# Optimization experiments

Hardware: AMD Instinct MI355X
Metric: run time of the kernel (lower is better)

Reference implementation:

```python
import jax, jax.numpy as jnp
import numpy as np

B, S, D, H = 16, 1024, 768, 12
HD = D // H  # head_dim = 64

def setup_inputs() -> dict:
    key = jax.random.key(0)
    ks = jax.random.split(key, 6)
    s = 1.0 / np.sqrt(D)
    return {
        "z": jax.random.normal(ks[0], (B, S, D), dtype=jnp.float32),
        "W_q": jax.random.normal(ks[1], (D, D), dtype=jnp.float32) * s,
        "W_k": jax.random.normal(ks[2], (D, D), dtype=jnp.float32) * s,
        "W_v": jax.random.normal(ks[3], (D, D), dtype=jnp.float32) * s,
        "W_o": jax.random.normal(ks[4], (D, D), dtype=jnp.float32) * s,
        "b_o": jax.random.normal(ks[5], (D,), dtype=jnp.float32) * s,
    }

def reference(z, W_q, W_k, W_v, W_o, b_o):
    batch, seq, _ = z.shape
    # torch Linear: y = x @ W.T
    q = (z @ W_q.T).reshape(batch, seq, H, HD).transpose(0, 2, 1, 3)  # [B,H,S,hd]
    k = (z @ W_k.T).reshape(batch, seq, H, HD).transpose(0, 2, 1, 3)
    v = (z @ W_v.T).reshape(batch, seq, H, HD).transpose(0, 2, 1, 3)
    scores = jnp.einsum("bhqd,bhkd->bhqk", q, k) / np.sqrt(HD)
    attn = jax.nn.softmax(scores, axis=-1)
    ctx = jnp.einsum("bhqk,bhkd->bhqd", attn, v)  # [B,H,S,hd]
    ctx = ctx.transpose(0, 2, 1, 3).reshape(batch, seq, D)
    return ctx @ W_o.T + b_o
```

## Files before the change

### kernel.cpp

```cpp
#include <hip/hip_runtime.h>
#include <hip/hip_bf16.h>


typedef __attribute__((ext_vector_type(4))) float f32x4;
typedef __attribute__((ext_vector_type(16))) float f32x16;
typedef __attribute__((ext_vector_type(8))) __bf16 bf16x8;
typedef __attribute__((ext_vector_type(4))) unsigned int u32x4;

#if __has_builtin(__builtin_amdgcn_exp2f)
#define EXP2F __builtin_amdgcn_exp2f
#else
#define EXP2F exp2f
#endif

__device__ __forceinline__ unsigned short f2bf(float f) {
  union { float f; unsigned u; } v; v.f = f;
  unsigned r = v.u + 0x7FFFu + ((v.u >> 16) & 1u);
  return (unsigned short)(r >> 16);
}

__device__ __forceinline__ unsigned cvtpk(float a, float b) {
  unsigned r;
  asm("v_cvt_pk_bf16_f32 %0, %1, %2" : "=v"(r) : "v"(a), "v"(b));
  return r;
}

__device__ __forceinline__ void gl_lds16(const void* g, void* l) {
  __builtin_amdgcn_global_load_lds(
      (const __attribute__((address_space(1))) void*)g,
      (__attribute__((address_space(3))) void*)l, 16, 0, 0);
}

__global__ void cvt_f32_bf16(const float* __restrict__ in,
                             unsigned short* __restrict__ out, int n4) {
  int i = blockIdx.x * blockDim.x + threadIdx.x;
  int stride = gridDim.x * blockDim.x;
  for (; i < n4; i += stride) {
    float4 v = ((const float4*)in)[i];
    ushort4 o;
    o.x = f2bf(v.x); o.y = f2bf(v.y); o.z = f2bf(v.z); o.w = f2bf(v.w);
    ((ushort4*)out)[i] = o;
  }
}

__global__ void cvt4_f32_bf16(const float* __restrict__ i0, const float* __restrict__ i1,
                              const float* __restrict__ i2, const float* __restrict__ i3,
                              unsigned short* __restrict__ o0, unsigned short* __restrict__ o1,
                              unsigned short* __restrict__ o2, unsigned short* __restrict__ o3,
                              int n4) {
  const float* in = (blockIdx.y == 0) ? i0 : (blockIdx.y == 1) ? i1 : (blockIdx.y == 2) ? i2 : i3;
  unsigned short* out = (blockIdx.y == 0) ? o0 : (blockIdx.y == 1) ? o1 : (blockIdx.y == 2) ? o2 : o3;
  int i = blockIdx.x * blockDim.x + threadIdx.x;
  int stride = gridDim.x * blockDim.x;
  for (; i < n4; i += stride) {
    float4 v = ((const float4*)in)[i];
    ushort4 o;
    o.x = f2bf(v.x); o.y = f2bf(v.y); o.z = f2bf(v.z); o.w = f2bf(v.w);
    ((ushort4*)out)[i] = o;
  }
}

__global__ __launch_bounds__(256) void qkv_gemm(
    const unsigned short* __restrict__ A,
    const unsigned short* __restrict__ Wq,
    const unsigned short* __restrict__ Wk,
    const unsigned short* __restrict__ Wv,
    unsigned short* __restrict__ Qo,
    unsigned short* __restrict__ Ko,
    unsigned short* __restrict__ Vt) {
  __shared__ unsigned short As[2][128 * 64];
  __shared__ unsigned short Bs[2][128 * 64];
  const int bid = blockIdx.x;
  const int xcd = bid & 7, slot = bid >> 3;
  const int mt = xcd * 16 + slot / 18;
  const int rem = slot % 18;
  const int which = rem / 6;
  const int nt = rem % 6;
  const unsigned short* __restrict__ W =
      (which == 0) ? Wq : (which == 1) ? Wk : Wv;
  const int m0 = mt * 128;
  const int n0 = nt * 128;
  const int tid = threadIdx.x;
  const int lane = tid & 63;
  const int l15 = lane & 15, lg = lane >> 4;
  const int w = tid >> 6;
  const int wm = (w >> 1) * 64, wn = (w & 1) * 64;

  const int srow = tid >> 3;
  const int scg8 = (((tid & 7) ^ (srow & 7)) << 3);

#define QSTAGE(bi, kt)                                                         \
  do {                                                                         \
    _Pragma("unroll") for (int it = 0; it < 4; ++it) {                         \
      int row = srow + it * 32;                                                \
      int dst = (row * 8 + (tid & 7)) * 8;                                     \
      gl_lds16(A + (size_t)(m0 + row) * 768 + (kt) + scg8, &As[bi][dst]);      \
      gl_lds16(W + (size_t)(n0 + row) * 768 + (kt) + scg8, &Bs[bi][dst]);      \
    }                                                                          \
  } while (0)

  f32x4 acc[4][4] = {};
  const int rxf = l15 & 7;

  QSTAGE(0, 0);
  for (int kt = 0; kt < 768; kt += 64) {
    const int cur = (kt >> 6) & 1;
    if (kt < 704) {
      QSTAGE(cur ^ 1, kt + 64);
      asm volatile("s_waitcnt vmcnt(8)" ::: "memory");
    } else {
      asm volatile("s_waitcnt vmcnt(0)" ::: "memory");
    }
    __builtin_amdgcn_s_barrier();
    __builtin_amdgcn_sched_barrier(0);
#pragma unroll
    for (int kk = 0; kk < 64; kk += 32) {
      const int g0 = kk >> 3;
      bf16x8 a[4], b[4];
#pragma unroll
      for (int i = 0; i < 4; ++i)
        a[i] = *(const bf16x8*)&As[cur][(wm + i * 16 + l15) * 64 + (((g0 + lg) ^ rxf) << 3)];
#pragma unroll
      for (int j = 0; j < 4; ++j)
        b[j] = *(const bf16x8*)&Bs[cur][(wn + j * 16 + l15) * 64 + (((g0 + lg) ^ rxf) << 3)];
#pragma unroll
      for (int i = 0; i < 4; ++i)
#pragma unroll
        for (int j = 0; j < 4; ++j)
          acc[i][j] = __builtin_amdgcn_mfma_f32_16x16x32_bf16(
              a[i], b[j], acc[i][j], 0, 0, 0);
    }
    asm volatile("s_waitcnt lgkmcnt(0)" ::: "memory");
    __builtin_amdgcn_sched_barrier(0);
    __builtin_amdgcn_s_barrier();
  }

  if (which < 2) {
    unsigned short* __restrict__ O = which == 0 ? Qo : Ko;
    const float scl = which == 0 ? 0.125f * 1.44269504088896f : 1.0f;
#pragma unroll
    for (int i = 0; i < 4; ++i)
#pragma unroll
      for (int j = 0; j < 4; ++j)
#pragma unroll
        for (int r = 0; r < 4; ++r) {
          int row = m0 + wm + i * 16 + lg * 4 + r;
          int col = n0 + wn + j * 16 + l15;
          O[(size_t)row * 768 + col] = f2bf(acc[i][j][r] * scl);
        }
  } else {
#pragma unroll
    for (int i = 0; i < 4; ++i)
#pragma unroll
      for (int j = 0; j < 4; ++j) {
        int m = m0 + wm + i * 16 + lg * 4;
        int bb = m >> 10, s = m & 1023;
        int col = n0 + wn + j * 16 + l15;
        size_t off = ((size_t)(bb * 12 + (col >> 6)) * 64 + (col & 63)) * 1024 + s;
        ushort4 pk;
        pk.x = f2bf(acc[i][j][0]);
        pk.y = f2bf(acc[i][j][1]);
        pk.z = f2bf(acc[i][j][2]);
        pk.w = f2bf(acc[i][j][3]);
        *(ushort4*)(Vt + off) = pk;
      }
  }
#undef QSTAGE
}

__global__ __launch_bounds__(256, 2) void attn_fwd(
    const unsigned short* __restrict__ Q,
    const unsigned short* __restrict__ K,
    const unsigned short* __restrict__ Vt,
    unsigned short* __restrict__ ctx) {
  __shared__ unsigned short Ks[2][64 * 64];
  __shared__ unsigned short Vs[2][64 * 64];
  const int wg = blockIdx.x;
  const int xcd = wg & 7, slot = wg >> 3;
  const int bh = xcd * 24 + (slot >> 2);
  const int qt = slot & 3;
  const int b = bh / 12, h = bh - b * 12;

  const int tid = threadIdx.x;
  const int lane = tid & 63;
  const int l31 = lane & 31;
  const int hi = lane >> 5;
  const int w = tid >> 6;
  const int qbase = qt * 256 + w * 64;

  const size_t qkoff = (size_t)b * (1024 * 768) + h * 64;
  const size_t vtoff = (size_t)bh * (64 * 1024);

  const int sc = lane & 7;
  const int srsub = lane >> 3;
  const int scg = sc ^ srsub;
  const int srow0 = w * 16 + srsub;

  const unsigned short* k0 = K + qkoff + scg * 8 + (size_t)srow0 * 768;
  const unsigned short* k1 = k0 + 8 * 768;
  const unsigned short* v0 = Vt + vtoff + scg * 8 + (size_t)srow0 * 1024;
  const unsigned short* v1 = v0 + 8 * 1024;
  const int d0 = srow0 * 64 + sc * 8;
  const int d1 = d0 + 8 * 64;

#define STAGE(bi)                                                              \
  do {                                                                         \
    gl_lds16(k0, &Ks[bi][d0]);                                                 \
    gl_lds16(k1, &Ks[bi][d1]);                                                 \
    gl_lds16(v0, &Vs[bi][d0]);                                                 \
    gl_lds16(v1, &Vs[bi][d1]);                                                 \
    k0 += 64 * 768; k1 += 64 * 768; v0 += 64; v1 += 64;                        \
  } while (0)

  bf16x8 bqA[4], bqB[4];
  const unsigned short* Qp = Q + qkoff + (size_t)(qbase + l31) * 768 + hi * 8;
#pragma unroll
  for (int ks = 0; ks < 4; ++ks) {
    bqA[ks] = *(const bf16x8*)(Qp + ks * 16);
    bqB[ks] = *(const bf16x8*)(Qp + 32 * 768 + ks * 16);
  }

  f32x16 oA0 = {}, oA1 = {}, oB0 = {}, oB1 = {};
  float laccA[8] = {}, laccB[8] = {};

  const int rxor = l31 & 7;

  STAGE(0);
  asm volatile("s_waitcnt vmcnt(0)");
  __syncthreads();

  for (int t = 0; t < 1024; t += 64) {
    const int cur = (t >> 6) & 1;
    if (t < 960) STAGE(cur ^ 1);

    bf16x8 ak[2][4], bv[2][4];
#pragma unroll
    for (int kb = 0; kb < 2; ++kb)
#pragma unroll
      for (int ks = 0; ks < 4; ++ks)
        ak[kb][ks] = *(const bf16x8*)&Ks[cur][(kb * 32 + l31) * 64 + (((ks * 2 + hi) ^ rxor) * 8)];
#pragma unroll
    for (int db = 0; db < 2; ++db)
#pragma unroll
      for (int ks = 0; ks < 4; ++ks)
        bv[db][ks] = *(const bf16x8*)&Vs[cur][(db * 32 + l31) * 64 + (((ks * 2 + hi) ^ rxor) * 8)];

    f32x16 sA0 = {}, sA1 = {}, sB0 = {}, sB1 = {};
    __builtin_amdgcn_s_setprio(1);
#pragma unroll
    for (int ks = 0; ks < 4; ++ks) {
      sA0 = __builtin_amdgcn_mfma_f32_32x32x16_bf16(ak[0][ks], bqA[ks], sA0, 0, 0, 0);
      sA1 = __builtin_amdgcn_mfma_f32_32x32x16_bf16(ak[1][ks], bqA[ks], sA1, 0, 0, 0);
    }
#pragma unroll
    for (int ks = 0; ks < 4; ++ks) {
      sB0 = __builtin_amdgcn_mfma_f32_32x32x16_bf16(ak[0][ks], bqB[ks], sB0, 0, 0, 0);
      sB1 = __builtin_amdgcn_mfma_f32_32x32x16_bf16(ak[1][ks], bqB[ks], sB1, 0, 0, 0);
    }
    __builtin_amdgcn_s_setprio(0);

#pragma unroll
    for (int r = 0; r < 16; ++r) sA0[r] = EXP2F(sA0[r]);
#pragma unroll
    for (int r = 0; r < 16; ++r) sA1[r] = EXP2F(sA1[r]);
#pragma unroll
    for (int r = 0; r < 8; ++r)
      laccA[r] += (sA0[r] + sA0[r + 8]) + (sA1[r] + sA1[r + 8]);

    bf16x8 pa[4];
#pragma unroll
    for (int ks = 0; ks < 4; ++ks) {
      f32x16 ps = (ks < 2) ? sA0 : sA1;
      const int roff = (ks & 1) * 8;
      unsigned c01 = cvtpk(ps[roff + 0], ps[roff + 1]);
      unsigned c23 = cvtpk(ps[roff + 2], ps[roff + 3]);
      unsigned c45 = cvtpk(ps[roff + 4], ps[roff + 5]);
      unsigned c67 = cvtpk(ps[roff + 6], ps[roff + 7]);
      unsigned e1 = hi ? c01 : c45;
      unsigned e2 = hi ? c23 : c67;
      unsigned se1 = (unsigned)__shfl_xor((int)e1, 32);
      unsigned se2 = (unsigned)__shfl_xor((int)e2, 32);
      u32x4 uw;
      uw[0] = hi ? se1 : c01;
      uw[1] = hi ? se2 : c23;
      uw[2] = hi ? c45 : se1;
      uw[3] = hi ? c67 : se2;
      pa[ks] = __builtin_bit_cast(bf16x8, uw);
    }
    __builtin_amdgcn_s_setprio(1);
#pragma unroll
    for (int ks = 0; ks < 4; ++ks) {
      oA0 = __builtin_amdgcn_mfma_f32_32x32x16_bf16(pa[ks], bv[0][ks], oA0, 0, 0, 0);
      oA1 = __builtin_amdgcn_mfma_f32_32x32x16_bf16(pa[ks], bv[1][ks], oA1, 0, 0, 0);
    }
    __builtin_amdgcn_s_setprio(0);

#pragma unroll
    for (int r = 0; r < 16; ++r) sB0[r] = EXP2F(sB0[r]);
#pragma unroll
    for (int r = 0; r < 16; ++r) sB1[r] = EXP2F(sB1[r]);
#pragma unroll
    for (int r = 0; r < 8; ++r)
      laccB[r] += (sB0[r] + sB0[r + 8]) + (sB1[r] + sB1[r + 8]);

#pragma unroll
    for (int ks = 0; ks < 4; ++ks) {
      f32x16 ps = (ks < 2) ? sB0 : sB1;
      const int roff = (ks & 1) * 8;
      unsigned c01 = cvtpk(ps[roff + 0], ps[roff + 1]);
      unsigned c23 = cvtpk(ps[roff + 2], ps[roff + 3]);
      unsigned c45 = cvtpk(ps[roff + 4], ps[roff + 5]);
      unsigned c67 = cvtpk(ps[roff + 6], ps[roff + 7]);
      unsigned e1 = hi ? c01 : c45;
      unsigned e2 = hi ? c23 : c67;
      unsigned se1 = (unsigned)__shfl_xor((int)e1, 32);
      unsigned se2 = (unsigned)__shfl_xor((int)e2, 32);
      u32x4 uw;
      uw[0] = hi ? se1 : c01;
      uw[1] = hi ? se2 : c23;
      uw[2] = hi ? c45 : se1;
      uw[3] = hi ? c67 : se2;
      pa[ks] = __builtin_bit_cast(bf16x8, uw);
    }
    __builtin_amdgcn_s_setprio(1);
#pragma unroll
    for (int ks = 0; ks < 4; ++ks) {
      oB0 = __builtin_amdgcn_mfma_f32_32x32x16_bf16(pa[ks], bv[0][ks], oB0, 0, 0, 0);
      oB1 = __builtin_amdgcn_mfma_f32_32x32x16_bf16(pa[ks], bv[1][ks], oB1, 0, 0, 0);
    }
    __builtin_amdgcn_s_setprio(0);

    asm volatile("s_waitcnt vmcnt(0)");
    __syncthreads();
  }

  unsigned short* Cp = ctx + qkoff;
  {
    float lsA = ((laccA[0] + laccA[1]) + (laccA[2] + laccA[3])) +
                ((laccA[4] + laccA[5]) + (laccA[6] + laccA[7]));
    lsA += __shfl_xor(lsA, 32);
    float invA = 1.0f / lsA;
#pragma unroll
    for (int r = 0; r < 16; ++r) {
      int qof = (r & 3) + 8 * (r >> 2) + 4 * hi;
      float invO = __shfl(invA, qof);
      size_t rowo = (size_t)(qbase + qof) * 768 + l31;
      Cp[rowo] = f2bf(oA0[r] * invO);
      Cp[rowo + 32] = f2bf(oA1[r] * invO);
    }
  }
  {
    float lsB = ((laccB[0] + laccB[1]) + (laccB[2] + laccB[3])) +
                ((laccB[4] + laccB[5]) + (laccB[6] + laccB[7]));
    lsB += __shfl_xor(lsB, 32);
    float invB = 1.0f / lsB;
#pragma unroll
    for (int r = 0; r < 16; ++r) {
      int qof = (r & 3) + 8 * (r >> 2) + 4 * hi;
      float invO = __shfl(invB, qof);
      size_t rowo = (size_t)(qbase + 32 + qof) * 768 + l31;
      Cp[rowo] = f2bf(oB0[r] * invO);
      Cp[rowo + 32] = f2bf(oB1[r] * invO);
    }
  }
#undef STAGE
}

__global__ __launch_bounds__(256) void oproj_gemm(
    const unsigned short* __restrict__ A,
    const unsigned short* __restrict__ W,
    const float* __restrict__ bias,
    float* __restrict__ out) {
  __shared__ unsigned short As[2][128 * 64];
  __shared__ unsigned short Bs[2][128 * 64];
  const int bid = blockIdx.x;
  const int xcd = bid & 7, slot = bid >> 3;
  const int mt = xcd * 16 + slot / 6;
  const int nt = slot % 6;
  const int m0 = mt * 128;
  const int n0 = nt * 128;
  const int tid = threadIdx.x;
  const int lane = tid & 63;
  const int l15 = lane & 15, lg = lane >> 4;
  const int w = tid >> 6;
  const int wm = (w >> 1) * 64, wn = (w & 1) * 64;

  const int srow = tid >> 3;
  const int scg8 = (((tid & 7) ^ (srow & 7)) << 3);

#define OSTAGE(bi, kt)                                                         \
  do {                                                                         \
    _Pragma("unroll") for (int it = 0; it < 4; ++it) {                         \
      int row = srow + it * 32;                                                \
      int dst = (row * 8 + (tid & 7)) * 8;                                     \
      gl_lds16(A + (size_t)(m0 + row) * 768 + (kt) + scg8, &As[bi][dst]);      \
      gl_lds16(W + (size_t)(n0 + row) * 768 + (kt) + scg8, &Bs[bi][dst]);      \
    }                                                                          \
  } while (0)

  f32x4 acc[4][4] = {};
  const int rxf = l15 & 7;

  OSTAGE(0, 0);
  for (int kt = 0; kt < 768; kt += 64) {
    const int cur = (kt >> 6) & 1;
    if (kt < 704) {
      OSTAGE(cur ^ 1, kt + 64);
      asm volatile("s_waitcnt vmcnt(8)" ::: "memory");
    } else {
      asm volatile("s_waitcnt vmcnt(0)" ::: "memory");
    }
    __builtin_amdgcn_s_barrier();
    __builtin_amdgcn_sched_barrier(0);
#pragma unroll
    for (int kk = 0; kk < 64; kk += 32) {
      const int g0 = kk >> 3;
      bf16x8 a[4], b[4];
#pragma unroll
      for (int i = 0; i < 4; ++i)
        a[i] = *(const bf16x8*)&As[cur][(wm + i * 16 + l15) * 64 + (((g0 + lg) ^ rxf) << 3)];
#pragma unroll
      for (int j = 0; j < 4; ++j)
        b[j] = *(const bf16x8*)&Bs[cur][(wn + j * 16 + l15) * 64 + (((g0 + lg) ^ rxf) << 3)];
#pragma unroll
      for (int i = 0; i < 4; ++i)
#pragma unroll
        for (int j = 0; j < 4; ++j)
          acc[i][j] = __builtin_amdgcn_mfma_f32_16x16x32_bf16(
              a[i], b[j], acc[i][j], 0, 0, 0);
    }
    asm volatile("s_waitcnt lgkmcnt(0)" ::: "memory");
    __builtin_amdgcn_sched_barrier(0);
    __builtin_amdgcn_s_barrier();
  }

#pragma unroll
  for (int i = 0; i < 4; ++i)
#pragma unroll
    for (int j = 0; j < 4; ++j)
#pragma unroll
      for (int r = 0; r < 4; ++r) {
        int row = m0 + wm + i * 16 + lg * 4 + r;
        int col = n0 + wn + j * 16 + l15;
        out[(size_t)row * 768 + col] = acc[i][j][r] + bias[col];
      }
#undef OSTAGE
}

extern "C" void kernel_launch(void* const* d_in, const int* in_sizes, int n_in,
                              void* d_out, int out_size, void* d_ws, size_t ws_size,
                              hipStream_t stream) {
  const float* z = (const float*)d_in[0];
  const float* Wq = (const float*)d_in[1];
  const float* Wk = (const float*)d_in[2];
  const float* Wv = (const float*)d_in[3];
  const float* Wo = (const float*)d_in[4];
  const float* bo = (const float*)d_in[5];
  float* out = (float*)d_out;

  const size_t NZ = (size_t)16 * 1024 * 768;
  const size_t NW = (size_t)768 * 768;

  unsigned short* zb = (unsigned short*)d_ws;
  unsigned short* Wqb = zb + NZ;
  unsigned short* Wkb = Wqb + NW;
  unsigned short* Wvb = Wkb + NW;
  unsigned short* Wob = Wvb + NW;
  unsigned short* Qb = Wob + NW;
  unsigned short* Kb = Qb + NZ;
  unsigned short* Vtb = Kb + NZ;
  unsigned short* Cb = Vtb + NZ;

  cvt_f32_bf16<<<2048, 256, 0, stream>>>(z, zb, (int)(NZ / 4));
  cvt4_f32_bf16<<<dim3(144, 4), 256, 0, stream>>>(Wq, Wk, Wv, Wo, Wqb, Wkb, Wvb, Wob,
                                                  (int)(NW / 4));

  qkv_gemm<<<2304, 256, 0, stream>>>(zb, Wqb, Wkb, Wvb, Qb, Kb, Vtb);
  attn_fwd<<<768, 256, 0, stream>>>(Qb, Kb, Vtb, Cb);
  oproj_gemm<<<768, 256, 0, stream>>>(Cb, Wob, bo, out);
}
```

Before: 183.6 us.

## Fuse z fp32-to-bf16 conversion into QKV GEMM and halve attention block size

Drops the separate z conversion kernel. The QKV GEMM now loads fp32 z into registers, packs it to bf16 with v_cvt_pk_bf16_f32, and writes it to LDS while the W tile still streams in through global_load_lds. This removes a full write and reread of the bf16 copy of z. Attention now runs 128-thread blocks with two waves each over 128 query rows, doubling the grid to 1536 blocks for better occupancy and load balance, at the cost of more K/V reloads per head. The register-staged A path adds VGPR pressure, and z is now read as fp32 once per N tile, i.e. 18 times.

```diff
diff --git a/kernel.cpp b/kernel.cpp
--- a/kernel.cpp
+++ b/kernel.cpp
@@ -29,18 +29,6 @@
   __builtin_amdgcn_global_load_lds(
       (const __attribute__((address_space(1))) void*)g,
       (__attribute__((address_space(3))) void*)l, 16, 0, 0);
-}
-
-__global__ void cvt_f32_bf16(const float* __restrict__ in,
-                             unsigned short* __restrict__ out, int n4) {
-  int i = blockIdx.x * blockDim.x + threadIdx.x;
-  int stride = gridDim.x * blockDim.x;
-  for (; i < n4; i += stride) {
-    float4 v = ((const float4*)in)[i];
-    ushort4 o;
-    o.x = f2bf(v.x); o.y = f2bf(v.y); o.z = f2bf(v.z); o.w = f2bf(v.w);
-    ((ushort4*)out)[i] = o;
-  }
 }
 
 __global__ void cvt4_f32_bf16(const float* __restrict__ i0, const float* __restrict__ i1,
@@ -61,7 +49,7 @@
 }
 
 __global__ __launch_bounds__(256) void qkv_gemm(
-    const unsigned short* __restrict__ A,
+    const float* __restrict__ Z,
     const unsigned short* __restrict__ Wq,
     const unsigned short* __restrict__ Wk,
     const unsigned short* __restrict__ Wv,
@@ -89,25 +77,53 @@
   const int srow = tid >> 3;
   const int scg8 = (((tid & 7) ^ (srow & 7)) << 3);
 
-#define QSTAGE(bi, kt)                                                         \
+  float4 ra[4][2];
+
+#define ALOAD(kt)                                                              \
+  do {                                                                         \
+    _Pragma("unroll") for (int it = 0; it < 4; ++it) {                         \
+      const float* p = Z + (size_t)(m0 + srow + it * 32) * 768 + (kt) + scg8;  \
+      ra[it][0] = *(const float4*)p;                                           \
+      ra[it][1] = *(const float4*)(p + 4);                                     \
+    }                                                                          \
+  } while (0)
+
+#define AWRITE(bi)                                                             \
+  do {                                                                         \
+    _Pragma("unroll") for (int it = 0; it < 4; ++it) {                         \
+      u32x4 pw;                                                                \
+      pw[0] = cvtpk(ra[it][0].x, ra[it][0].y);                                 \
+      pw[1] = cvtpk(ra[it][0].z, ra[it][0].w);                                 \
+      pw[2] = cvtpk(ra[it][1].x, ra[it][1].y);                                 \
+      pw[3] = cvtpk(ra[it][1].z, ra[it][1].w);                                 \
+      *(u32x4*)&As[bi][(((srow + it * 32) * 8 + (tid & 7)) * 8)] = pw;         \
+    }                                                                          \
+  } while (0)
+
+#define WSTAGE(bi, kt)                                                         \
   do {                                                                         \
     _Pragma("unroll") for (int it = 0; it < 4; ++it) {                         \
       int row = srow + it * 32;                                                \
-      int dst = (row * 8 + (tid & 7)) * 8;                                     \
-      gl_lds16(A + (size_t)(m0 + row) * 768 + (kt) + scg8, &As[bi][dst]);      \
-      gl_lds16(W + (size_t)(n0 + row) * 768 + (kt) + scg8, &Bs[bi][dst]);      \
+      gl_lds16(W + (size_t)(n0 + row) * 768 + (kt) + scg8,                     \
+               &Bs[bi][(row * 8 + (tid & 7)) * 8]);                            \
     }                                                                          \
   } while (0)
 
   f32x4 acc[4][4] = {};
   const int rxf = l15 & 7;
 
-  QSTAGE(0, 0);
+  ALOAD(0);
+  WSTAGE(0, 0);
+  asm volatile("s_waitcnt vmcnt(4)" ::: "memory");
+  AWRITE(0);
+  asm volatile("s_waitcnt lgkmcnt(0)" ::: "memory");
+
   for (int kt = 0; kt < 768; kt += 64) {
     const int cur = (kt >> 6) & 1;
     if (kt < 704) {
-      QSTAGE(cur ^ 1, kt + 64);
-      asm volatile("s_waitcnt vmcnt(8)" ::: "memory");
+      ALOAD(kt + 64);
+      WSTAGE(cur ^ 1, kt + 64);
+      asm volatile("s_waitcnt vmcnt(12)" ::: "memory");
     } else {
       asm volatile("s_waitcnt vmcnt(0)" ::: "memory");
     }
@@ -129,6 +145,10 @@
         for (int j = 0; j < 4; ++j)
           acc[i][j] = __builtin_amdgcn_mfma_f32_16x16x32_bf16(
               a[i], b[j], acc[i][j], 0, 0, 0);
+    }
+    if (kt < 704) {
+      asm volatile("s_waitcnt vmcnt(4)" ::: "memory");
+      AWRITE(cur ^ 1);
     }
     asm volatile("s_waitcnt lgkmcnt(0)" ::: "memory");
     __builtin_amdgcn_sched_barrier(0);
@@ -165,10 +185,12 @@
         *(ushort4*)(Vt + off) = pk;
       }
   }
-#undef QSTAGE
-}
-
-__global__ __launch_bounds__(256, 2) void attn_fwd(
+#undef ALOAD
+#undef AWRITE
+#undef WSTAGE
+}
+
+__global__ __launch_bounds__(128, 2) void attn_fwd(
     const unsigned short* __restrict__ Q,
     const unsigned short* __restrict__ K,
     const unsigned short* __restrict__ Vt,
@@ -177,8 +199,8 @@
   __shared__ unsigned short Vs[2][64 * 64];
   const int wg = blockIdx.x;
   const int xcd = wg & 7, slot = wg >> 3;
-  const int bh = xcd * 24 + (slot >> 2);
-  const int qt = slot & 3;
+  const int bh = xcd * 24 + (slot >> 3);
+  const int qt = slot & 7;
   const int b = bh / 12, h = bh - b * 12;
 
   const int tid = threadIdx.x;
@@ -186,7 +208,7 @@
   const int l31 = lane & 31;
   const int hi = lane >> 5;
   const int w = tid >> 6;
-  const int qbase = qt * 256 + w * 64;
+  const int qbase = qt * 128 + w * 64;
 
   const size_t qkoff = (size_t)b * (1024 * 768) + h * 64;
   const size_t vtoff = (size_t)bh * (64 * 1024);
@@ -194,22 +216,19 @@
   const int sc = lane & 7;
   const int srsub = lane >> 3;
   const int scg = sc ^ srsub;
-  const int srow0 = w * 16 + srsub;
-
-  const unsigned short* k0 = K + qkoff + scg * 8 + (size_t)srow0 * 768;
-  const unsigned short* k1 = k0 + 8 * 768;
-  const unsigned short* v0 = Vt + vtoff + scg * 8 + (size_t)srow0 * 1024;
-  const unsigned short* v1 = v0 + 8 * 1024;
-  const int d0 = srow0 * 64 + sc * 8;
-  const int d1 = d0 + 8 * 64;
+  const int srow0 = w * 32 + srsub;
+
+  const unsigned short* kb = K + qkoff + scg * 8 + (size_t)srow0 * 768;
+  const unsigned short* vb = Vt + vtoff + scg * 8 + (size_t)srow0 * 1024;
+  const int dbase = srow0 * 64 + sc * 8;
 
 #define STAGE(bi)                                                              \
   do {                                                                         \
-    gl_lds16(k0, &Ks[bi][d0]);                                                 \
-    gl_lds16(k1, &Ks[bi][d1]);                                                 \
-    gl_lds16(v0, &Vs[bi][d0]);                                                 \
-    gl_lds16(v1, &Vs[bi][d1]);                                                 \
-    k0 += 64 * 768; k1 += 64 * 768; v0 += 64; v1 += 64;                        \
+    _Pragma("unroll") for (int j = 0; j < 4; ++j) {                            \
+      gl_lds16(kb + (size_t)j * (8 * 768), &Ks[bi][dbase + j * (8 * 64)]);     \
+      gl_lds16(vb + (size_t)j * (8 * 1024), &Vs[bi][dbase + j * (8 * 64)]);    \
+    }                                                                          \
+    kb += 64 * 768; vb += 64;                                                  \
   } while (0)
 
   bf16x8 bqA[4], bqB[4];
@@ -235,10 +254,10 @@
 
     bf16x8 ak[2][4], bv[2][4];
 #pragma unroll
-    for (int kb = 0; kb < 2; ++kb)
+    for (int kb2 = 0; kb2 < 2; ++kb2)
 #pragma unroll
       for (int ks = 0; ks < 4; ++ks)
-        ak[kb][ks] = *(const bf16x8*)&Ks[cur][(kb * 32 + l31) * 64 + (((ks * 2 + hi) ^ rxor) * 8)];
+        ak[kb2][ks] = *(const bf16x8*)&Ks[cur][(kb2 * 32 + l31) * 64 + (((ks * 2 + hi) ^ rxor) * 8)];
 #pragma unroll
     for (int db = 0; db < 2; ++db)
 #pragma unroll
@@ -461,8 +480,7 @@
   const size_t NZ = (size_t)16 * 1024 * 768;
   const size_t NW = (size_t)768 * 768;
 
-  unsigned short* zb = (unsigned short*)d_ws;
-  unsigned short* Wqb = zb + NZ;
+  unsigned short* Wqb = (unsigned short*)d_ws;
   unsigned short* Wkb = Wqb + NW;
   unsigned short* Wvb = Wkb + NW;
   unsigned short* Wob = Wvb + NW;
@@ -471,11 +489,10 @@
   unsigned short* Vtb = Kb + NZ;
   unsigned short* Cb = Vtb + NZ;
 
-  cvt_f32_bf16<<<2048, 256, 0, stream>>>(z, zb, (int)(NZ / 4));
   cvt4_f32_bf16<<<dim3(144, 4), 256, 0, stream>>>(Wq, Wk, Wv, Wo, Wqb, Wkb, Wvb, Wob,
                                                   (int)(NW / 4));
 
-  qkv_gemm<<<2304, 256, 0, stream>>>(zb, Wqb, Wkb, Wvb, Qb, Kb, Vtb);
-  attn_fwd<<<768, 256, 0, stream>>>(Qb, Kb, Vtb, Cb);
+  qkv_gemm<<<2304, 256, 0, stream>>>(z, Wqb, Wkb, Wvb, Qb, Kb, Vtb);
+  attn_fwd<<<1536, 128, 0, stream>>>(Qb, Kb, Vtb, Cb);
   oproj_gemm<<<768, 256, 0, stream>>>(Cb, Wob, bo, out);
 }
```

After: 213.6 us. 1.16x slower.

## Deepen attention K/V pipeline to four LDS buffers with two-tile steps

Applied to the files above, without the earlier changes.

The attention kernel's K/V shared-memory staging goes from double to quadruple buffering. Each loop iteration now processes two 64-key tiles while prefetching the next two, and waits with a partial vmcnt so loads stay in flight across compute. The goal is fewer barriers per key and better hiding of global-to-LDS latency. LDS per block doubles to 64KB, which may limit the two-blocks-per-CU occupancy, and the hand-written vmcnt count must match the number of loads STAGE issues.

```diff
diff --git a/kernel.cpp b/kernel.cpp
--- a/kernel.cpp
+++ b/kernel.cpp
@@ -173,8 +173,8 @@
     const unsigned short* __restrict__ K,
     const unsigned short* __restrict__ Vt,
     unsigned short* __restrict__ ctx) {
-  __shared__ unsigned short Ks[2][64 * 64];
-  __shared__ unsigned short Vs[2][64 * 64];
+  __shared__ unsigned short Ks[4][64 * 64];
+  __shared__ unsigned short Vs[4][64 * 64];
   const int wg = blockIdx.x;
   const int xcd = wg & 7, slot = wg >> 3;
   const int bh = xcd * 24 + (slot >> 2);
@@ -225,113 +225,109 @@
 
   const int rxor = l31 & 7;
 
+#define ATTN_BODY(buf)                                                         \
+  do {                                                                         \
+    bf16x8 ak[2][4], bv[2][4];                                                 \
+    _Pragma("unroll") for (int kb2 = 0; kb2 < 2; ++kb2)                        \
+      _Pragma("unroll") for (int ks = 0; ks < 4; ++ks)                         \
+        ak[kb2][ks] = *(const bf16x8*)&Ks[buf][(kb2 * 32 + l31) * 64 +         \
+                                               (((ks * 2 + hi) ^ rxor) * 8)];  \
+    _Pragma("unroll") for (int db = 0; db < 2; ++db)                           \
+      _Pragma("unroll") for (int ks = 0; ks < 4; ++ks)                         \
+        bv[db][ks] = *(const bf16x8*)&Vs[buf][(db * 32 + l31) * 64 +           \
+                                              (((ks * 2 + hi) ^ rxor) * 8)];   \
+    f32x16 sA0 = {}, sA1 = {}, sB0 = {}, sB1 = {};                             \
+    __builtin_amdgcn_s_setprio(1);                                             \
+    _Pragma("unroll") for (int ks = 0; ks < 4; ++ks) {                         \
+      sA0 = __builtin_amdgcn_mfma_f32_32x32x16_bf16(ak[0][ks], bqA[ks], sA0, 0, 0, 0); \
+      sA1 = __builtin_amdgcn_mfma_f32_32x32x16_bf16(ak[1][ks], bqA[ks], sA1, 0, 0, 0); \
+    }                                                                          \
+    _Pragma("unroll") for (int ks = 0; ks < 4; ++ks) {                         \
+      sB0 = __builtin_amdgcn_mfma_f32_32x32x16_bf16(ak[0][ks], bqB[ks], sB0, 0, 0, 0); \
+      sB1 = __builtin_amdgcn_mfma_f32_32x32x16_bf16(ak[1][ks], bqB[ks], sB1, 0, 0, 0); \
+    }                                                                          \
+    __builtin_amdgcn_s_setprio(0);                                             \
+    _Pragma("unroll") for (int r = 0; r < 16; ++r) sA0[r] = EXP2F(sA0[r]);     \
+    _Pragma("unroll") for (int r = 0; r < 16; ++r) sA1[r] = EXP2F(sA1[r]);     \
+    _Pragma("unroll") for (int r = 0; r < 8; ++r)                              \
+      laccA[r] += (sA0[r] + sA0[r + 8]) + (sA1[r] + sA1[r + 8]);               \
+    bf16x8 pa[4];                                                              \
+    _Pragma("unroll") for (int ks = 0; ks < 4; ++ks) {                         \
+      f32x16 ps = (ks < 2) ? sA0 : sA1;                                        \
+      const int roff = (ks & 1) * 8;                                           \
+      unsigned c01 = cvtpk(ps[roff + 0], ps[roff + 1]);                        \
+      unsigned c23 = cvtpk(ps[roff + 2], ps[roff + 3]);                        \
+      unsigned c45 = cvtpk(ps[roff + 4], ps[roff + 5]);                        \
+      unsigned c67 = cvtpk(ps[roff + 6], ps[roff + 7]);                        \
+      unsigned e1 = hi ? c01 : c45;                                            \
+      unsigned e2 = hi ? c23 : c67;                                            \
+      unsigned se1 = (unsigned)__shfl_xor((int)e1, 32);                        \
+      unsigned se2 = (unsigned)__shfl_xor((int)e2, 32);                        \
+      u32x4 uw;                                                                \
+      uw[0] = hi ? se1 : c01;                                                  \
+      uw[1] = hi ? se2 : c23;                                                  \
+      uw[2] = hi ? c45 : se1;                                                  \
+      uw[3] = hi ? c67 : se2;                                                  \
+      pa[ks] = __builtin_bit_cast(bf16x8, uw);                                 \
+    }                                                                          \
+    __builtin_amdgcn_s_setprio(1);                                             \
+    _Pragma("unroll") for (int ks = 0; ks < 4; ++ks) {                         \
+      oA0 = __builtin_amdgcn_mfma_f32_32x32x16_bf16(pa[ks], bv[0][ks], oA0, 0, 0, 0); \
+      oA1 = __builtin_amdgcn_mfma_f32_32x32x16_bf16(pa[ks], bv[1][ks], oA1, 0, 0, 0); \
+    }                                                                          \
+    __builtin_amdgcn_s_setprio(0);                                             \
+    _Pragma("unroll") for (int r = 0; r < 16; ++r) sB0[r] = EXP2F(sB0[r]);     \
+    _Pragma("unroll") for (int r = 0; r < 16; ++r) sB1[r] = EXP2F(sB1[r]);     \
+    _Pragma("unroll") for (int r = 0; r < 8; ++r)                              \
+      laccB[r] += (sB0[r] + sB0[r + 8]) + (sB1[r] + sB1[r + 8]);               \
+    _Pragma("unroll") for (int ks = 0; ks < 4; ++ks) {                         \
+      f32x16 ps = (ks < 2) ? sB0 : sB1;                                        \
+      const int roff = (ks & 1) * 8;                                           \
+      unsigned c01 = cvtpk(ps[roff + 0], ps[roff + 1]);                        \
+      unsigned c23 = cvtpk(ps[roff + 2], ps[roff + 3]);                        \
+      unsigned c45 = cvtpk(ps[roff + 4], ps[roff + 5]);                        \
+      unsigned c67 = cvtpk(ps[roff + 6], ps[roff + 7]);                        \
+      unsigned e1 = hi ? c01 : c45;                                            \
+      unsigned e2 = hi ? c23 : c67;                                            \
+      unsigned se1 = (unsigned)__shfl_xor((int)e1, 32);                        \
+      unsigned se2 = (unsigned)__shfl_xor((int)e2, 32);                        \
+      u32x4 uw;                                                                \
+      uw[0] = hi ? se1 : c01;                                                  \
+      uw[1] = hi ? se2 : c23;                                                  \
+      uw[2] = hi ? c45 : se1;                                                  \
+      uw[3] = hi ? c67 : se2;                                                  \
+      pa[ks] = __builtin_bit_cast(bf16x8, uw);                                 \
+    }                                                                          \
+    __builtin_amdgcn_s_setprio(1);                                             \
+    _Pragma("unroll") for (int ks = 0; ks < 4; ++ks) {                         \
+      oB0 = __builtin_amdgcn_mfma_f32_32x32x16_bf16(pa[ks], bv[0][ks], oB0, 0, 0, 0); \
+      oB1 = __builtin_amdgcn_mfma_f32_32x32x16_bf16(pa[ks], bv[1][ks], oB1, 0, 0, 0); \
+    }                                                                          \
+    __builtin_amdgcn_s_setprio(0);                                             \
+  } while (0)
+
   STAGE(0);
-  asm volatile("s_waitcnt vmcnt(0)");
-  __syncthreads();
-
-  for (int t = 0; t < 1024; t += 64) {
-    const int cur = (t >> 6) & 1;
-    if (t < 960) STAGE(cur ^ 1);
-
-    bf16x8 ak[2][4], bv[2][4];
-#pragma unroll
-    for (int kb = 0; kb < 2; ++kb)
-#pragma unroll
-      for (int ks = 0; ks < 4; ++ks)
-        ak[kb][ks] = *(const bf16x8*)&Ks[cur][(kb * 32 + l31) * 64 + (((ks * 2 + hi) ^ rxor) * 8)];
-#pragma unroll
-    for (int db = 0; db < 2; ++db)
-#pragma unroll
-      for (int ks = 0; ks < 4; ++ks)
-        bv[db][ks] = *(const bf16x8*)&Vs[cur][(db * 32 + l31) * 64 + (((ks * 2 + hi) ^ rxor) * 8)];
-
-    f32x16 sA0 = {}, sA1 = {}, sB0 = {}, sB1 = {};
-    __builtin_amdgcn_s_setprio(1);
-#pragma unroll
-    for (int ks = 0; ks < 4; ++ks) {
-      sA0 = __builtin_amdgcn_mfma_f32_32x32x16_bf16(ak[0][ks], bqA[ks], sA0, 0, 0, 0);
-      sA1 = __builtin_amdgcn_mfma_f32_32x32x16_bf16(ak[1][ks], bqA[ks], sA1, 0, 0, 0);
-    }
-#pragma unroll
-    for (int ks = 0; ks < 4; ++ks) {
-      sB0 = __builtin_amdgcn_mfma_f32_32x32x16_bf16(ak[0][ks], bqB[ks], sB0, 0, 0, 0);
-      sB1 = __builtin_amdgcn_mfma_f32_32x32x16_bf16(ak[1][ks], bqB[ks], sB1, 0, 0, 0);
-    }
-    __builtin_amdgcn_s_setprio(0);
-
-#pragma unroll
-    for (int r = 0; r < 16; ++r) sA0[r] = EXP2F(sA0[r]);
-#pragma unroll
-    for (int r = 0; r < 16; ++r) sA1[r] = EXP2F(sA1[r]);
-#pragma unroll
-    for (int r = 0; r < 8; ++r)
-      laccA[r] += (sA0[r] + sA0[r + 8]) + (sA1[r] + sA1[r + 8]);
-
-    bf16x8 pa[4];
-#pragma unroll
-    for (int ks = 0; ks < 4; ++ks) {
-      f32x16 ps = (ks < 2) ? sA0 : sA1;
-      const int roff = (ks & 1) * 8;
-      unsigned c01 = cvtpk(ps[roff + 0], ps[roff + 1]);
-      unsigned c23 = cvtpk(ps[roff + 2], ps[roff + 3]);
-      unsigned c45 = cvtpk(ps[roff + 4], ps[roff + 5]);
-      unsigned c67 = cvtpk(ps[roff + 6], ps[roff + 7]);
-      unsigned e1 = hi ? c01 : c45;
-      unsigned e2 = hi ? c23 : c67;
-      unsigned se1 = (unsigned)__shfl_xor((int)e1, 32);
-      unsigned se2 = (unsigned)__shfl_xor((int)e2, 32);
-      u32x4 uw;
-      uw[0] = hi ? se1 : c01;
-      uw[1] = hi ? se2 : c23;
-      uw[2] = hi ? c45 : se1;
-      uw[3] = hi ? c67 : se2;
-      pa[ks] = __builtin_bit_cast(bf16x8, uw);
-    }
-    __builtin_amdgcn_s_setprio(1);
-#pragma unroll
-    for (int ks = 0; ks < 4; ++ks) {
-      oA0 = __builtin_amdgcn_mfma_f32_32x32x16_bf16(pa[ks], bv[0][ks], oA0, 0, 0, 0);
-      oA1 = __builtin_amdgcn_mfma_f32_32x32x16_bf16(pa[ks], bv[1][ks], oA1, 0, 0, 0);
-    }
-    __builtin_amdgcn_s_setprio(0);
-
-#pragma unroll
-    for (int r = 0; r < 16; ++r) sB0[r] = EXP2F(sB0[r]);
-#pragma unroll
-    for (int r = 0; r < 16; ++r) sB1[r] = EXP2F(sB1[r]);
-#pragma unroll
-    for (int r = 0; r < 8; ++r)
-      laccB[r] += (sB0[r] + sB0[r + 8]) + (sB1[r] + sB1[r + 8]);
-
-#pragma unroll
-    for (int ks = 0; ks < 4; ++ks) {
-      f32x16 ps = (ks < 2) ? sB0 : sB1;
-      const int roff = (ks & 1) * 8;
-      unsigned c01 = cvtpk(ps[roff + 0], ps[roff + 1]);
-      unsigned c23 = cvtpk(ps[roff + 2], ps[roff + 3]);
-      unsigned c45 = cvtpk(ps[roff + 4], ps[roff + 5]);
-      unsigned c67 = cvtpk(ps[roff + 6], ps[roff + 7]);
-      unsigned e1 = hi ? c01 : c45;
-      unsigned e2 = hi ? c23 : c67;
-      unsigned se1 = (unsigned)__shfl_xor((int)e1, 32);
-      unsigned se2 = (unsigned)__shfl_xor((int)e2, 32);
-      u32x4 uw;
-      uw[0] = hi ? se1 : c01;
-      uw[1] = hi ? se2 : c23;
-      uw[2] = hi ? c45 : se1;
-      uw[3] = hi ? c67 : se2;
-      pa[ks] = __builtin_bit_cast(bf16x8, uw);
-    }
-    __builtin_amdgcn_s_setprio(1);
-#pragma unroll
-    for (int ks = 0; ks < 4; ++ks) {
-      oB0 = __builtin_amdgcn_mfma_f32_32x32x16_bf16(pa[ks], bv[0][ks], oB0, 0, 0, 0);
-      oB1 = __builtin_amdgcn_mfma_f32_32x32x16_bf16(pa[ks], bv[1][ks], oB1, 0, 0, 0);
-    }
-    __builtin_amdgcn_s_setprio(0);
-
-    asm volatile("s_waitcnt vmcnt(0)");
-    __syncthreads();
+  STAGE(1);
+
+#pragma unroll 1
+  for (int i = 0; i < 8; ++i) {
+    const int cur0 = (i & 1) * 2;
+    if (i < 7) {
+      STAGE(cur0 ^ 2);
+      STAGE((cur0 ^ 2) + 1);
+      asm volatile("s_waitcnt vmcnt(8)" ::: "memory");
+    } else {
+      asm volatile("s_waitcnt vmcnt(0)" ::: "memory");
+    }
+    __builtin_amdgcn_s_barrier();
+    __builtin_amdgcn_sched_barrier(0);
+
+    ATTN_BODY(cur0);
+    ATTN_BODY(cur0 + 1);
+
+    asm volatile("s_waitcnt lgkmcnt(0)" ::: "memory");
+    __builtin_amdgcn_sched_barrier(0);
+    __builtin_amdgcn_s_barrier();
   }
 
   unsigned short* Cp = ctx + qkoff;
@@ -364,6 +360,7 @@
     }
   }
 #undef STAGE
+#undef ATTN_BODY
 }
 
 __global__ __launch_bounds__(256) void oproj_gemm(
```

After: 184.3 us. Within noise of the previous version (+0.4%).
